# Optimization experiments

Measured on AMD Instinct MI355X. Metric: run time of the kernel, lower is better.

The kernel has to match this reference:

```python
import jax, jax.numpy as jnp
import numpy as np

INPUT_DIM = 1024
HIDDEN = 1024
NUM_EXPERTS = 64
TOP_K = 8
N_TOKENS = 32768


def _linear_params(key, fan_in, fan_out):
    kw, kb = jax.random.split(key)
    bound = 1.0 / np.sqrt(fan_in)
    w = jax.random.uniform(kw, (fan_in, fan_out), jnp.float32, -bound, bound)
    b = jax.random.uniform(kb, (fan_out,), jnp.float32, -bound, bound)
    return w, b


def setup_inputs() -> dict:
    key = jax.random.key(0)
    ks = jax.random.split(key, 8)
    x = jax.random.normal(ks[0], (N_TOKENS, INPUT_DIM), jnp.float32)
    noise = jax.random.normal(ks[1], (N_TOKENS, NUM_EXPERTS), jnp.float32)
    h2 = 2 * HIDDEN
    w1, b1 = _linear_params(ks[2], INPUT_DIM, h2)
    w2, b2 = _linear_params(ks[3], h2, h2)
    wn, bn = _linear_params(ks[4], h2, h2)
    w3, b3 = _linear_params(ks[5], h2, HIDDEN)
    w4, b4 = _linear_params(ks[6], HIDDEN, NUM_EXPERTS)
    wz, bz = _linear_params(ks[7], INPUT_DIM, NUM_EXPERTS)
    return {"x": x, "noise": noise, "w1": w1, "b1": b1, "w2": w2, "b2": b2,
            "wn": wn, "bn": bn, "w3": w3, "b3": b3, "w4": w4, "b4": b4,
            "wz": wz, "bz": bz}


def reference(x, noise, w1, b1, w2, b2, wn, bn, w3, b3, w4, b4, wz, bz):
    relu = jax.nn.relu
    h = relu(x @ w1 + b1)            # [N, 2H]
    h = relu(h @ w2 + b2)            # [N, 2H]
    h = relu(h @ wn + bn)            # [N, 2H]
    h = relu(h @ w3 + b3)            # [N, H]
    logits = h @ w4 + b4             # [N, E]
    noise_logits = x @ wz + bz       # [N, E]
    noisy_logits = logits + noise * jax.nn.softplus(noise_logits)
    top_k_logits, indices = jax.lax.top_k(noisy_logits, TOP_K)  # [N, K]
    rows = jnp.arange(noisy_logits.shape[0])[:, None]
    sparse_logits = jnp.full_like(noisy_logits, -jnp.inf).at[rows, indices].set(top_k_logits)
    router_output = jax.nn.softmax(sparse_logits, axis=-1)      # [N, E]
    return router_output, indices
```

## Files before the change

kernel.cpp:

```cpp
#include <hip/hip_runtime.h>
#include <math.h>

#define IN_DIM 1024
#define H2     2048
#define HID    1024
#define NEXP   64
#define TOPK   8
#define RISK_TH 1.5e-4f

typedef short  v8s __attribute__((ext_vector_type(8)));
typedef float  v4f __attribute__((ext_vector_type(4)));

__device__ __forceinline__ void bf16_split(float f, ushort& h, ushort& l) {
    unsigned uh = __float_as_uint(f) & 0xffff0000u;
    h = (ushort)(uh >> 16);
    float r = f - __uint_as_float(uh);
    l = (ushort)(__float_as_uint(r) >> 16);
}

__device__ __forceinline__ void gload16(const ushort* g, ushort* l) {
    __builtin_amdgcn_global_load_lds(
        (const __attribute__((address_space(1))) void*)g,
        (__attribute__((address_space(3))) void*)l, 16, 0, 0);
}

__global__ __launch_bounds__(256)
void split_w_kernel(const float* __restrict__ W, ushort* __restrict__ hiT,
                    ushort* __restrict__ loT, int K, int N)
{
    __shared__ float T[64][65];
    const int k0 = blockIdx.y * 64, n0 = blockIdx.x * 64;
    const int t = threadIdx.x;
#pragma unroll
    for (int j = 0; j < 4; ++j) {
        int idx = t + j * 256;
        int row = idx >> 4;
        int c4  = (idx & 15) * 4;
        float4 f = *(const float4*)(W + (long)(k0 + row) * N + n0 + c4);
        T[row][c4 + 0] = f.x; T[row][c4 + 1] = f.y;
        T[row][c4 + 2] = f.z; T[row][c4 + 3] = f.w;
    }
    __syncthreads();
#pragma unroll
    for (int j = 0; j < 4; ++j) {
        int idx = t + j * 256;
        int nn = idx >> 4;
        int kq = (idx & 15) * 4;
        ushort4 h4, l4;
        bf16_split(T[kq + 0][nn], h4.x, l4.x);
        bf16_split(T[kq + 1][nn], h4.y, l4.y);
        bf16_split(T[kq + 2][nn], h4.z, l4.z);
        bf16_split(T[kq + 3][nn], h4.w, l4.w);
        long o = (long)(n0 + nn) * K + k0 + kq;
        *(ushort4*)(hiT + o) = h4;
        *(ushort4*)(loT + o) = l4;
    }
}

__global__ __launch_bounds__(256)
void split_x_kernel(const float* __restrict__ X, ushort* __restrict__ hi,
                    ushort* __restrict__ lo)
{
    long i = ((long)blockIdx.x * 256 + threadIdx.x) * 4;
    float4 f = *(const float4*)(X + i);
    ushort4 h4, l4;
    bf16_split(f.x, h4.x, l4.x);
    bf16_split(f.y, h4.y, l4.y);
    bf16_split(f.z, h4.z, l4.z);
    bf16_split(f.w, h4.w, l4.w);
    *(ushort4*)(hi + i) = h4;
    *(ushort4*)(lo + i) = l4;
}

template<int MI, int NWN>
__global__ __launch_bounds__(512, 2)
void gemm8p_kernel(const ushort* __restrict__ gAhi, const ushort* __restrict__ gAlo,
                   const ushort* __restrict__ gBhi, const ushort* __restrict__ gBlo,
                   const float* __restrict__ bias,
                   float* __restrict__ Cf32, ushort* __restrict__ Chi,
                   ushort* __restrict__ Clo, int N, int K)
{
    static_assert(MI == 2 * NWN, "wave grid must tile 256 rows");
    constexpr int BN    = NWN * 64;
    constexpr int ATILE = 256 * 32;
    constexpr int BTILE = BN * 32;
    constexpr int BUFU  = 2 * ATILE + 2 * BTILE;
    constexpr int MH    = MI / 2;
    __shared__ __align__(16) ushort lds[2 * BUFU];

    const int tid  = threadIdx.x;
    const int w    = tid >> 6;
    const int lane = tid & 63;
    const int wm   = w / NWN;
    const int wn   = w % NWN;
    const int q    = lane >> 4;
    const int l15  = lane & 15;

    const int nwg = (int)(gridDim.x * gridDim.y);
    const int h   = (int)(blockIdx.y * gridDim.x + blockIdx.x);
    const int l   = (h & 7) * (nwg >> 3) + (h >> 3);
    const long bm = (long)(l >> 3) * 256;
    const long bn = (long)(l & 7) * BN;

    const int  e   = lane >> 2;
    const int  s8  = (((lane & 3) ^ ((lane >> 3) & 3)) * 8);
    const int  fragUS = ((q ^ ((l15 >> 1) & 3)) * 8);

    const int NT = K >> 5;

    v4f acc[MI][4];
#pragma unroll
    for (int mi = 0; mi < MI; ++mi)
#pragma unroll
        for (int ni = 0; ni < 4; ++ni)
            acc[mi][ni] = (v4f){0.f, 0.f, 0.f, 0.f};

    {
        ushort* nb = lds;
        const long grA = bm + w * 16 + e;
        gload16(gAhi + grA * K + s8,                     nb + w * 512);
        gload16(gAhi + (grA + 128) * K + s8,             nb + 128 * 32 + w * 512);
        gload16(gAlo + grA * K + s8,                     nb + ATILE + w * 512);
        gload16(gAlo + (grA + 128) * K + s8,             nb + ATILE + 128 * 32 + w * 512);
        const long grB = bn + w * 16 + e;
        gload16(gBhi + grB * K + s8,                     nb + 2 * ATILE + w * 512);
        gload16(gBlo + grB * K + s8,                     nb + 2 * ATILE + BTILE + w * 512);
        if constexpr (BN == 256) {
            gload16(gBhi + (grB + 128) * K + s8,         nb + 2 * ATILE + 128 * 32 + w * 512);
            gload16(gBlo + (grB + 128) * K + s8,         nb + 2 * ATILE + BTILE + 128 * 32 + w * 512);
        }
    }
    asm volatile("s_waitcnt vmcnt(0)" ::: "memory");
    __builtin_amdgcn_s_barrier();

    for (int t = 0; t < NT; ++t) {
        const ushort* cA = lds + (t & 1) * BUFU;
        const ushort* cB = cA + 2 * ATILE;
        ushort* nb = lds + ((t + 1) & 1) * BUFU;
        const bool more = (t + 1 < NT);
        const int  ktn  = (t + 1) << 5;

        v8s ah[MH], al[MH];
        v8s bh0[2], bl0[2];
        v8s bh1[2], bl1[2];

#pragma unroll
        for (int i = 0; i < MH; ++i) {
            int r = wm * (MI * 16) + i * 16 + l15;
            const ushort* pA = cA + r * 32 + fragUS;
            ah[i] = *(const v8s*)pA;
            al[i] = *(const v8s*)(pA + ATILE);
        }
#pragma unroll
        for (int j = 0; j < 2; ++j) {
            int r = wn * 64 + j * 16 + l15;
            const ushort* pB = cB + r * 32 + fragUS;
            bh0[j] = *(const v8s*)pB;
            bl0[j] = *(const v8s*)(pB + BTILE);
        }
        if (more) {
            const long gr = bm + w * 16 + e;
            gload16(gAhi + gr * K + ktn + s8,             nb + w * 512);
            gload16(gAhi + (gr + 128) * K + ktn + s8,     nb + 128 * 32 + w * 512);
            gload16(gAlo + gr * K + ktn + s8,             nb + ATILE + w * 512);
            gload16(gAlo + (gr + 128) * K + ktn + s8,     nb + ATILE + 128 * 32 + w * 512);
        }
        asm volatile("s_waitcnt lgkmcnt(0)" ::: "memory");
        __builtin_amdgcn_sched_barrier(0);

#pragma unroll
        for (int j = 0; j < 2; ++j) {
            int r = wn * 64 + (2 + j) * 16 + l15;
            const ushort* pB = cB + r * 32 + fragUS;
            bh1[j] = *(const v8s*)pB;
            bl1[j] = *(const v8s*)(pB + BTILE);
        }

        __builtin_amdgcn_s_setprio(1);
#pragma unroll
        for (int i = 0; i < MH; ++i)
#pragma unroll
            for (int j = 0; j < 2; ++j) {
                v4f c = acc[i][j];
                c = __builtin_amdgcn_mfma_f32_16x16x32_bf16(al[i], bh0[j], c, 0, 0, 0);
                c = __builtin_amdgcn_mfma_f32_16x16x32_bf16(ah[i], bl0[j], c, 0, 0, 0);
                c = __builtin_amdgcn_mfma_f32_16x16x32_bf16(ah[i], bh0[j], c, 0, 0, 0);
                acc[i][j] = c;
            }
        __builtin_amdgcn_s_setprio(0);

        if (more) {
            const long gr = bn + w * 16 + e;
            gload16(gBhi + gr * K + ktn + s8,             nb + 2 * ATILE + w * 512);
            gload16(gBlo + gr * K + ktn + s8,             nb + 2 * ATILE + BTILE + w * 512);
            if constexpr (BN == 256) {
                gload16(gBhi + (gr + 128) * K + ktn + s8, nb + 2 * ATILE + 128 * 32 + w * 512);
                gload16(gBlo + (gr + 128) * K + ktn + s8, nb + 2 * ATILE + BTILE + 128 * 32 + w * 512);
            }
        }
        asm volatile("s_waitcnt lgkmcnt(0)" ::: "memory");
        __builtin_amdgcn_sched_barrier(0);

        __builtin_amdgcn_s_setprio(1);
#pragma unroll
        for (int i = 0; i < MH; ++i)
#pragma unroll
            for (int j = 0; j < 2; ++j) {
                v4f c = acc[i][2 + j];
                c = __builtin_amdgcn_mfma_f32_16x16x32_bf16(al[i], bh1[j], c, 0, 0, 0);
                c = __builtin_amdgcn_mfma_f32_16x16x32_bf16(ah[i], bl1[j], c, 0, 0, 0);
                c = __builtin_amdgcn_mfma_f32_16x16x32_bf16(ah[i], bh1[j], c, 0, 0, 0);
                acc[i][2 + j] = c;
            }
        __builtin_amdgcn_s_setprio(0);

#pragma unroll
        for (int i = 0; i < MH; ++i) {
            int r = wm * (MI * 16) + (MH + i) * 16 + l15;
            const ushort* pA = cA + r * 32 + fragUS;
            ah[i] = *(const v8s*)pA;
            al[i] = *(const v8s*)(pA + ATILE);
        }
        asm volatile("s_waitcnt lgkmcnt(0)" ::: "memory");
        __builtin_amdgcn_sched_barrier(0);

        __builtin_amdgcn_s_setprio(1);
#pragma unroll
        for (int i = 0; i < MH; ++i)
#pragma unroll
            for (int j = 0; j < 2; ++j) {
                v4f c = acc[MH + i][2 + j];
                c = __builtin_amdgcn_mfma_f32_16x16x32_bf16(al[i], bh1[j], c, 0, 0, 0);
                c = __builtin_amdgcn_mfma_f32_16x16x32_bf16(ah[i], bl1[j], c, 0, 0, 0);
                c = __builtin_amdgcn_mfma_f32_16x16x32_bf16(ah[i], bh1[j], c, 0, 0, 0);
                acc[MH + i][2 + j] = c;
            }
#pragma unroll
        for (int i = 0; i < MH; ++i)
#pragma unroll
            for (int j = 0; j < 2; ++j) {
                v4f c = acc[MH + i][j];
                c = __builtin_amdgcn_mfma_f32_16x16x32_bf16(al[i], bh0[j], c, 0, 0, 0);
                c = __builtin_amdgcn_mfma_f32_16x16x32_bf16(ah[i], bl0[j], c, 0, 0, 0);
                c = __builtin_amdgcn_mfma_f32_16x16x32_bf16(ah[i], bh0[j], c, 0, 0, 0);
                acc[MH + i][j] = c;
            }
        __builtin_amdgcn_s_setprio(0);

        asm volatile("s_waitcnt vmcnt(0)" ::: "memory");
        __builtin_amdgcn_s_barrier();
    }

#pragma unroll
    for (int ni = 0; ni < 4; ++ni) {
        int col = (int)(bn + wn * 64 + ni * 16 + l15);
        float bv = bias[col];
#pragma unroll
        for (int mi = 0; mi < MI; ++mi) {
            long row0 = bm + wm * (MI * 16) + mi * 16 + q * 4;
#pragma unroll
            for (int r = 0; r < 4; ++r) {
                float v = fmaxf(acc[mi][ni][r] + bv, 0.f);
                long o = (row0 + r) * (long)N + col;
                if (Cf32) {
                    Cf32[o] = v;
                } else {
                    ushort hh, ll;
                    bf16_split(v, hh, ll);
                    Chi[o] = hh;
                    Clo[o] = ll;
                }
            }
        }
    }
}

#define SBM 64
#define SBK 32
#define SLDA 68

__global__ __launch_bounds__(256, 2)
void small_gemm_kernel(const float* __restrict__ A, const float* __restrict__ B,
                       const float* __restrict__ bias, float* __restrict__ C,
                       int K)
{
    __shared__ __align__(16) float Hs[SBK][SLDA];
    __shared__ __align__(16) float Ws[SBK][NEXP];
    const int tid = threadIdx.x;
    const int tx = tid & 15;
    const int ty = tid >> 4;
    const long bm = (long)blockIdx.x * SBM;
    const float* Ab = A + bm * K;

    float acc[4][4];
#pragma unroll
    for (int i = 0; i < 4; ++i)
#pragma unroll
        for (int j = 0; j < 4; ++j) acc[i][j] = 0.f;

    float4 aR[2], bR[2];
#pragma unroll
    for (int j = 0; j < 2; ++j) {
        int idx = tid + (j << 8);
        int ar = idx >> 3, ac = (idx & 7) << 2;
        aR[j] = *(const float4*)(Ab + (long)ar * K + ac);
        int br = idx >> 4, bc = (idx & 15) << 2;
        bR[j] = *(const float4*)(B + (long)br * NEXP + bc);
    }

    int kt = 0;
    for (;;) {
#pragma unroll
        for (int j = 0; j < 2; ++j) {
            int idx = tid + (j << 8);
            int ar = idx >> 3, ac = (idx & 7) << 2;
            Hs[ac + 0][ar] = aR[j].x;
            Hs[ac + 1][ar] = aR[j].y;
            Hs[ac + 2][ar] = aR[j].z;
            Hs[ac + 3][ar] = aR[j].w;
            int br = idx >> 4, bc = (idx & 15) << 2;
            *(float4*)&Ws[br][bc] = bR[j];
        }
        __syncthreads();

        kt += SBK;
        if (kt < K) {
#pragma unroll
            for (int j = 0; j < 2; ++j) {
                int idx = tid + (j << 8);
                int ar = idx >> 3, ac = (idx & 7) << 2;
                aR[j] = *(const float4*)(Ab + (long)ar * K + kt + ac);
                int br = idx >> 4, bc = (idx & 15) << 2;
                bR[j] = *(const float4*)(B + (long)(kt + br) * NEXP + bc);
            }
        }

#pragma unroll
        for (int k = 0; k < SBK; ++k) {
            float a[4], b[4];
            *(float4*)&a[0] = *(const float4*)&Hs[k][ty * 4];
            *(float4*)&b[0] = *(const float4*)&Ws[k][tx * 4];
#pragma unroll
            for (int i = 0; i < 4; ++i)
#pragma unroll
                for (int j = 0; j < 4; ++j)
                    acc[i][j] = fmaf(a[i], b[j], acc[i][j]);
        }
        __syncthreads();
        if (kt >= K) break;
    }

    float bv[4];
#pragma unroll
    for (int j = 0; j < 4; ++j) bv[j] = bias[tx * 4 + j];
#pragma unroll
    for (int i = 0; i < 4; ++i) {
        long row = bm + ty * 4 + i;
        float o[4];
#pragma unroll
        for (int j = 0; j < 4; ++j) o[j] = acc[i][j] + bv[j];
        *(float4*)(C + row * NEXP + tx * 4) = *(const float4*)&o[0];
    }
}

__global__ __launch_bounds__(256)
void router_kernel(const float* __restrict__ logits, const float* __restrict__ nlog,
                   const float* __restrict__ noise, float* __restrict__ rout,
                   float* __restrict__ idx_out, int rows, int rowBase,
                   int* __restrict__ ctrl, int* __restrict__ list, int maxr)
{
    const int wave = threadIdx.x >> 6;
    const int lane = threadIdx.x & 63;
    const long row = (long)blockIdx.x * 4 + wave;
    if (row >= rows) return;

    float lg = logits[row * NEXP + lane];
    float nl = nlog[row * NEXP + lane];
    float nz = noise[row * NEXP + lane];
    float sp = fmaxf(nl, 0.f) + log1pf(expf(-fabsf(nl)));
    float v  = lg + nz * sp;

    float orig = v;
    float work = v;
    bool  sel  = false;
    float myidx = 0.f;
    float m = 0.f, ssum = 0.f;
    float prev = 0.f, minGap = INFINITY;

#pragma unroll
    for (int r = 0; r < TOPK + 1; ++r) {
        float bvv = work;
        int   bi  = lane;
#pragma unroll
        for (int off = 32; off > 0; off >>= 1) {
            float ov = __shfl_xor(bvv, off);
            int   oi = __shfl_xor(bi, off);
            if (ov > bvv || (ov == bvv && oi < bi)) { bvv = ov; bi = oi; }
        }
        if (r > 0) minGap = fminf(minGap, prev - bvv);
        prev = bvv;
        if (r < TOPK) {
            if (r == 0) m = bvv;
            ssum += expf(bvv - m);
            if (lane == bi) { work = -INFINITY; sel = true; }
            if (lane == r)  myidx = (float)bi;
        }
    }

    float p = sel ? expf(orig - m) / ssum : 0.f;
    rout[row * NEXP + lane] = p;
    if (lane < TOPK) idx_out[row * TOPK + lane] = myidx;

    if (lane == 0 && minGap < RISK_TH) {
        int slot = atomicAdd(ctrl, 1);
        if (slot < maxr) list[slot] = rowBase + (int)row;
    }
}

__global__ void init_kernel(int* ctrl) { if (threadIdx.x == 0) ctrl[0] = 0; }

__global__ void pad_kernel(int* ctrl, int* list, int maxr)
{
    int cnt = ctrl[0]; if (cnt > maxr) cnt = maxr;
    int rounded = (cnt + 63) & ~63; if (rounded > maxr) rounded = maxr;
    if (threadIdx.x == 0) { ctrl[1] = rounded; ctrl[2] = cnt; }
    int fill = (cnt > 0) ? list[0] : 0;
    for (int i = cnt + threadIdx.x; i < rounded; i += blockDim.x) list[i] = fill;
}

#define DBM 64
#define DBN 64
#define DBK 32

__global__ __launch_bounds__(256)
void dgemm_f64(const double* __restrict__ A64, const float* __restrict__ A32,
               const int* __restrict__ rowList,
               const float* __restrict__ B, const float* __restrict__ bias,
               double* __restrict__ C, int N, int K, int doRelu,
               const int* __restrict__ ctrl)
{
    const int mBase = blockIdx.y * DBM;
    if (mBase >= ctrl[1]) return;

    __shared__ __align__(16) double As[DBM][DBK + 2];
    __shared__ __align__(16) double Bs[DBK][DBN];
    __shared__ int rowIdx[DBM];

    const int tid = threadIdx.x;
    const int tx = tid & 15;
    const int ty = tid >> 4;
    const int nBase = blockIdx.x * DBN;

    if (A32 && tid < DBM) rowIdx[tid] = rowList[mBase + tid];
    __syncthreads();

    const int ar = tid >> 4;
    const int ak = (tid & 15) * 2;
    const int bc = (tid & 15) * 4;

    int rIdx[4];
    if (A32) {
#pragma unroll
        for (int j = 0; j < 4; ++j) rIdx[j] = rowIdx[ar + j * 16];
    }

    double acc[4][4];
#pragma unroll
    for (int i = 0; i < 4; ++i)
#pragma unroll
        for (int j = 0; j < 4; ++j) acc[i][j] = 0.0;

    double2 aReg[4];
    float4  bReg[2];

#pragma unroll
    for (int j = 0; j < 4; ++j) {
        if (A32) {
            const float2 f = *(const float2*)(A32 + (long)rIdx[j] * K + ak);
            aReg[j].x = (double)f.x; aReg[j].y = (double)f.y;
        } else {
            aReg[j] = *(const double2*)(A64 + (long)(mBase + ar + j * 16) * K + ak);
        }
    }
#pragma unroll
    for (int j = 0; j < 2; ++j)
        bReg[j] = *(const float4*)(B + (long)(ar + j * 16) * N + nBase + bc);

    int kt = 0;
    for (;;) {
#pragma unroll
        for (int j = 0; j < 4; ++j)
            *(double2*)&As[ar + j * 16][ak] = aReg[j];
#pragma unroll
        for (int j = 0; j < 2; ++j) {
            double2 lo, hi;
            lo.x = (double)bReg[j].x; lo.y = (double)bReg[j].y;
            hi.x = (double)bReg[j].z; hi.y = (double)bReg[j].w;
            *(double2*)&Bs[ar + j * 16][bc]     = lo;
            *(double2*)&Bs[ar + j * 16][bc + 2] = hi;
        }
        __syncthreads();

        kt += DBK;
        if (kt < K) {
#pragma unroll
            for (int j = 0; j < 4; ++j) {
                if (A32) {
                    const float2 f = *(const float2*)(A32 + (long)rIdx[j] * K + kt + ak);
                    aReg[j].x = (double)f.x; aReg[j].y = (double)f.y;
                } else {
                    aReg[j] = *(const double2*)(A64 + (long)(mBase + ar + j * 16) * K + kt + ak);
                }
            }
#pragma unroll
            for (int j = 0; j < 2; ++j)
                bReg[j] = *(const float4*)(B + (long)(kt + ar + j * 16) * N + nBase + bc);
        }

#pragma unroll
        for (int k = 0; k < DBK; ++k) {
            double a[4], b[4];
#pragma unroll
            for (int i = 0; i < 4; ++i) a[i] = As[ty * 4 + i][k];
            *(double2*)&b[0] = *(const double2*)&Bs[k][tx * 4];
            *(double2*)&b[2] = *(const double2*)&Bs[k][tx * 4 + 2];
#pragma unroll
            for (int i = 0; i < 4; ++i)
#pragma unroll
                for (int j = 0; j < 4; ++j)
                    acc[i][j] = fma(a[i], b[j], acc[i][j]);
        }
        __syncthreads();
        if (kt >= K) break;
    }

#pragma unroll
    for (int i = 0; i < 4; ++i) {
        long row = mBase + ty * 4 + i;
#pragma unroll
        for (int j = 0; j < 4; ++j) {
            int n = nBase + tx * 4 + j;
            double v = acc[i][j] + (double)bias[n];
            if (doRelu) v = fmax(v, 0.0);
            C[row * N + n] = v;
        }
    }
}

__global__ __launch_bounds__(256)
void router_fix_kernel(const double* __restrict__ lgd, const double* __restrict__ nld,
                       const float* __restrict__ noise, float* __restrict__ rout,
                       float* __restrict__ idx_out,
                       const int* __restrict__ ctrl, const int* __restrict__ list)
{
    const int wave = threadIdx.x >> 6;
    const int lane = threadIdx.x & 63;
    const int i = blockIdx.x * 4 + wave;
    if (i >= ctrl[2]) return;
    const long row = list[i];

    double lg = lgd[(long)i * NEXP + lane];
    double nl = nld[(long)i * NEXP + lane];
    double nz = (double)noise[row * NEXP + lane];
    double sp = fmax(nl, 0.0) + log1p(exp(-fabs(nl)));
    double v  = lg + nz * sp;

    double orig = v, work = v;
    bool sel = false;
    float myidx = 0.f;
    double m = 0.0, ssum = 0.0;

#pragma unroll
    for (int r = 0; r < TOPK; ++r) {
        double bvv = work;
        int    bi  = lane;
#pragma unroll
        for (int off = 32; off > 0; off >>= 1) {
            double ov = __shfl_xor(bvv, off);
            int    oi = __shfl_xor(bi, off);
            if (ov > bvv || (ov == bvv && oi < bi)) { bvv = ov; bi = oi; }
        }
        if (r == 0) m = bvv;
        ssum += exp(bvv - m);
        if (lane == bi) { work = -INFINITY; sel = true; }
        if (lane == r)  myidx = (float)bi;
    }

    double p = sel ? exp(orig - m) / ssum : 0.0;
    rout[row * NEXP + lane] = (float)p;
    if (lane < TOPK) idx_out[row * TOPK + lane] = myidx;
}

extern "C" void kernel_launch(void* const* d_in, const int* in_sizes, int n_in,
                              void* d_out, int out_size, void* d_ws, size_t ws_size,
                              hipStream_t stream)
{
    const float* x     = (const float*)d_in[0];
    const float* noise = (const float*)d_in[1];
    const float* w1 = (const float*)d_in[2];
    const float* b1 = (const float*)d_in[3];
    const float* w2 = (const float*)d_in[4];
    const float* b2 = (const float*)d_in[5];
    const float* wn = (const float*)d_in[6];
    const float* bn = (const float*)d_in[7];
    const float* w3 = (const float*)d_in[8];
    const float* b3 = (const float*)d_in[9];
    const float* w4 = (const float*)d_in[10];
    const float* b4 = (const float*)d_in[11];
    const float* wz = (const float*)d_in[12];
    const float* bz = (const float*)d_in[13];
    float* out = (float*)d_out;

    const int Ntok = in_sizes[0] / IN_DIM;

    const size_t e1 = (size_t)IN_DIM * H2;
    const size_t e2 = (size_t)H2 * H2;
    const size_t en = (size_t)H2 * H2;
    const size_t e3 = (size_t)H2 * HID;
    size_t weightBytes = 2 * (e1 + e2 + en + e3) * sizeof(ushort);
    weightBytes = (weightBytes + 255) & ~(size_t)255;

    const size_t perTok = (size_t)4 * H2 * 2 + (size_t)IN_DIM * 4 + 2 * NEXP * 4;
    int chunk = 8192;
    while (chunk > 256) {
        size_t needb = weightBytes + (size_t)chunk * perTok + 65536;
        if (needb <= ws_size) break;
        chunk >>= 1;
    }
    if (chunk > Ntok) chunk = Ntok;

    int MAXR = chunk / 2;
    if (MAXR > 4096) MAXR = 4096;

    ushort* w1Thi = (ushort*)d_ws;
    ushort* w1Tlo = w1Thi + e1;
    ushort* w2Thi = w1Tlo + e1;
    ushort* w2Tlo = w2Thi + e2;
    ushort* wnThi = w2Tlo + e2;
    ushort* wnTlo = wnThi + en;
    ushort* w3Thi = wnTlo + en;
    ushort* w3Tlo = w3Thi + e3;

    char* region = (char*)d_ws + weightBytes;
    const size_t regionBytes = (size_t)chunk * perTok;

    ushort* pAhi = (ushort*)region;
    ushort* pAlo = pAhi + (size_t)chunk * H2;
    ushort* pBhi = pAlo + (size_t)chunk * H2;
    ushort* pBlo = pBhi + (size_t)chunk * H2;
    char*   ureg = (char*)(pBlo + (size_t)chunk * H2);
    ushort* xphi = (ushort*)ureg;
    ushort* xplo = xphi + (size_t)chunk * IN_DIM;
    float*  hfin = (float*)ureg;
    float*  lg   = (float*)(ureg + (size_t)chunk * IN_DIM * 4);
    float*  nl   = lg + (size_t)chunk * NEXP;

    double* hA  = (double*)region;
    double* hB  = hA + (size_t)MAXR * H2;
    double* lgd = hB + (size_t)MAXR * H2;
    double* nld = lgd + (size_t)MAXR * NEXP;

    int* ctrl = (int*)(region + regionBytes);
    int* list = ctrl + 16;

    float* ridx = out + (size_t)Ntok * NEXP;

    const dim3 blk(256);
    init_kernel<<<1, 64, 0, stream>>>(ctrl);

    split_w_kernel<<<dim3(H2 / 64,  IN_DIM / 64), blk, 0, stream>>>(w1, w1Thi, w1Tlo, IN_DIM, H2);
    split_w_kernel<<<dim3(H2 / 64,  H2 / 64),     blk, 0, stream>>>(w2, w2Thi, w2Tlo, H2, H2);
    split_w_kernel<<<dim3(H2 / 64,  H2 / 64),     blk, 0, stream>>>(wn, wnThi, wnTlo, H2, H2);
    split_w_kernel<<<dim3(HID / 64, H2 / 64),     blk, 0, stream>>>(w3, w3Thi, w3Tlo, H2, HID);

    for (int c0 = 0; c0 < Ntok; c0 += chunk) {
        const float* xa = x + (size_t)c0 * IN_DIM;
        split_x_kernel<<<dim3(chunk), blk, 0, stream>>>(xa, xphi, xplo);
        gemm8p_kernel<8, 4><<<dim3(H2 / 256,  chunk / 256), 512, 0, stream>>>(
            xphi, xplo, w1Thi, w1Tlo, b1, nullptr, pAhi, pAlo, H2, IN_DIM);
        gemm8p_kernel<8, 4><<<dim3(H2 / 256,  chunk / 256), 512, 0, stream>>>(
            pAhi, pAlo, w2Thi, w2Tlo, b2, nullptr, pBhi, pBlo, H2, H2);
        gemm8p_kernel<8, 4><<<dim3(H2 / 256,  chunk / 256), 512, 0, stream>>>(
            pBhi, pBlo, wnThi, wnTlo, bn, nullptr, pAhi, pAlo, H2, H2);
        gemm8p_kernel<4, 2><<<dim3(HID / 128, chunk / 256), 512, 0, stream>>>(
            pAhi, pAlo, w3Thi, w3Tlo, b3, hfin, nullptr, nullptr, HID, H2);
        small_gemm_kernel<<<dim3(chunk / SBM), blk, 0, stream>>>(hfin, w4, b4, lg, HID);
        small_gemm_kernel<<<dim3(chunk / SBM), blk, 0, stream>>>(xa,   wz, bz, nl, IN_DIM);
        router_kernel<<<dim3(chunk / 4), blk, 0, stream>>>(lg, nl, noise + (size_t)c0 * NEXP,
                                                           out + (size_t)c0 * NEXP,
                                                           ridx + (size_t)c0 * TOPK, chunk, c0,
                                                           ctrl, list, MAXR);
    }

    pad_kernel<<<1, 256, 0, stream>>>(ctrl, list, MAXR);

    const dim3 gy(H2 / DBN, MAXR / DBM);
    dgemm_f64<<<gy, blk, 0, stream>>>(nullptr, x, list, w1, b1, hA, H2, IN_DIM, 1, ctrl);
    dgemm_f64<<<gy, blk, 0, stream>>>(hA, nullptr, nullptr, w2, b2, hB, H2, H2, 1, ctrl);
    dgemm_f64<<<gy, blk, 0, stream>>>(hB, nullptr, nullptr, wn, bn, hA, H2, H2, 1, ctrl);
    dgemm_f64<<<dim3(HID / DBN, MAXR / DBM), blk, 0, stream>>>(hA, nullptr, nullptr, w3, b3, hB, HID, H2, 1, ctrl);
    dgemm_f64<<<dim3(1, MAXR / DBM), blk, 0, stream>>>(hB, nullptr, nullptr, w4, b4, lgd, NEXP, HID, 0, ctrl);
    dgemm_f64<<<dim3(1, MAXR / DBM), blk, 0, stream>>>(nullptr, x, list, wz, bz, nld, NEXP, IN_DIM, 0, ctrl);
    router_fix_kernel<<<dim3(MAXR / 4), blk, 0, stream>>>(lgd, nld, noise, out, ridx, ctrl, list);
}
```

Baseline: 3.620 ms.

## Split-K the FP64 fix-up GEMMs with atomic accumulation and separate bias/ReLU pass

The double-precision re-computation path for risky rows now splits the K dimension across blockIdx.z and accumulates partial products into zeroed outputs with atomic adds. Bias and ReLU move into a separate fixzero kernel that also zeroes the next layer's output buffer, and the last-layer biases are folded into router_fix. The aim is more blocks in flight, since only a few rows are risky and the M-dimension grid is small. The cost is extra atomic traffic, extra kernel launches, and results that are not bitwise deterministic. The B fragment read in shared memory also changes from a contiguous double2 pattern to strided scalar reads.

```diff
diff --git a/kernel.cpp b/kernel.cpp
--- a/kernel.cpp
+++ b/kernel.cpp
@@ -428,19 +428,52 @@
     for (int i = cnt + threadIdx.x; i < rounded; i += blockDim.x) list[i] = fill;
 }
 
+__global__ __launch_bounds__(256)
+void fixzero_kernel(double* P, const float* __restrict__ bias, int cols,
+                    double* Z, int zcols, const int* __restrict__ ctrl)
+{
+    const int rp = blockIdx.y * 64;
+    if (rp >= ctrl[1]) return;
+    const int c0 = blockIdx.x * 64;
+    if (P && c0 < cols) {
+#pragma unroll
+        for (int i = 0; i < 8; ++i) {
+            int idx = threadIdx.x + i * 256;
+            int row = idx >> 5;
+            int col = (idx & 31) * 2;
+            long o = (long)(rp + row) * cols + c0 + col;
+            double2 v = *(double2*)(P + o);
+            v.x = fmax(v.x + (double)bias[c0 + col],     0.0);
+            v.y = fmax(v.y + (double)bias[c0 + col + 1], 0.0);
+            *(double2*)(P + o) = v;
+        }
+    }
+    if (Z && c0 < zcols) {
+        const double2 z2 = {0.0, 0.0};
+#pragma unroll
+        for (int i = 0; i < 8; ++i) {
+            int idx = threadIdx.x + i * 256;
+            int row = idx >> 5;
+            int col = (idx & 31) * 2;
+            *(double2*)(Z + (long)(rp + row) * zcols + c0 + col) = z2;
+        }
+    }
+}
+
 #define DBM 64
 #define DBN 64
 #define DBK 32
 
 __global__ __launch_bounds__(256)
-void dgemm_f64(const double* __restrict__ A64, const float* __restrict__ A32,
-               const int* __restrict__ rowList,
-               const float* __restrict__ B, const float* __restrict__ bias,
-               double* __restrict__ C, int N, int K, int doRelu,
-               const int* __restrict__ ctrl)
+void dgemm_ks(const double* __restrict__ A64, const float* __restrict__ A32,
+              const int* __restrict__ rowList,
+              const float* __restrict__ B, double* __restrict__ C,
+              int N, int K, int kLen, const int* __restrict__ ctrl)
 {
     const int mBase = blockIdx.y * DBM;
     if (mBase >= ctrl[1]) return;
+    const int kBase = blockIdx.z * kLen;
+    const int kEnd  = kBase + kLen;
 
     __shared__ __align__(16) double As[DBM][DBK + 2];
     __shared__ __align__(16) double Bs[DBK][DBN];
@@ -473,20 +506,23 @@
     double2 aReg[4];
     float4  bReg[2];
 
-#pragma unroll
-    for (int j = 0; j < 4; ++j) {
-        if (A32) {
-            const float2 f = *(const float2*)(A32 + (long)rIdx[j] * K + ak);
-            aReg[j].x = (double)f.x; aReg[j].y = (double)f.y;
-        } else {
-            aReg[j] = *(const double2*)(A64 + (long)(mBase + ar + j * 16) * K + ak);
-        }
-    }
-#pragma unroll
-    for (int j = 0; j < 2; ++j)
-        bReg[j] = *(const float4*)(B + (long)(ar + j * 16) * N + nBase + bc);
-
-    int kt = 0;
+    auto prefetch = [&](int ktv) {
+#pragma unroll
+        for (int j = 0; j < 4; ++j) {
+            if (A32) {
+                const float2 f = *(const float2*)(A32 + (long)rIdx[j] * K + ktv + ak);
+                aReg[j].x = (double)f.x; aReg[j].y = (double)f.y;
+            } else {
+                aReg[j] = *(const double2*)(A64 + (long)(mBase + ar + j * 16) * K + ktv + ak);
+            }
+        }
+#pragma unroll
+        for (int j = 0; j < 2; ++j)
+            bReg[j] = *(const float4*)(B + (long)(ktv + ar + j * 16) * N + nBase + bc);
+    };
+
+    prefetch(kBase);
+    int kt = kBase;
     for (;;) {
 #pragma unroll
         for (int j = 0; j < 4; ++j)
@@ -502,28 +538,15 @@
         __syncthreads();
 
         kt += DBK;
-        if (kt < K) {
-#pragma unroll
-            for (int j = 0; j < 4; ++j) {
-                if (A32) {
-                    const float2 f = *(const float2*)(A32 + (long)rIdx[j] * K + kt + ak);
-                    aReg[j].x = (double)f.x; aReg[j].y = (double)f.y;
-                } else {
-                    aReg[j] = *(const double2*)(A64 + (long)(mBase + ar + j * 16) * K + kt + ak);
-                }
-            }
-#pragma unroll
-            for (int j = 0; j < 2; ++j)
-                bReg[j] = *(const float4*)(B + (long)(kt + ar + j * 16) * N + nBase + bc);
-        }
+        if (kt < kEnd) prefetch(kt);
 
 #pragma unroll
         for (int k = 0; k < DBK; ++k) {
             double a[4], b[4];
 #pragma unroll
             for (int i = 0; i < 4; ++i) a[i] = As[ty * 4 + i][k];
-            *(double2*)&b[0] = *(const double2*)&Bs[k][tx * 4];
-            *(double2*)&b[2] = *(const double2*)&Bs[k][tx * 4 + 2];
+#pragma unroll
+            for (int j = 0; j < 4; ++j) b[j] = Bs[k][tx + j * 16];
 #pragma unroll
             for (int i = 0; i < 4; ++i)
 #pragma unroll
@@ -531,7 +554,7 @@
                     acc[i][j] = fma(a[i], b[j], acc[i][j]);
         }
         __syncthreads();
-        if (kt >= K) break;
+        if (kt >= kEnd) break;
     }
 
 #pragma unroll
@@ -539,16 +562,19 @@
         long row = mBase + ty * 4 + i;
 #pragma unroll
         for (int j = 0; j < 4; ++j) {
-            int n = nBase + tx * 4 + j;
-            double v = acc[i][j] + (double)bias[n];
-            if (doRelu) v = fmax(v, 0.0);
-            C[row * N + n] = v;
+            int n = nBase + tx + j * 16;
+#if defined(__HIP_PLATFORM_AMD__)
+            unsafeAtomicAdd(&C[row * N + n], acc[i][j]);
+#else
+            atomicAdd(&C[row * N + n], acc[i][j]);
+#endif
         }
     }
 }
 
 __global__ __launch_bounds__(256)
 void router_fix_kernel(const double* __restrict__ lgd, const double* __restrict__ nld,
+                       const float* __restrict__ b4f, const float* __restrict__ bzf,
                        const float* __restrict__ noise, float* __restrict__ rout,
                        float* __restrict__ idx_out,
                        const int* __restrict__ ctrl, const int* __restrict__ list)
@@ -559,8 +585,8 @@
     if (i >= ctrl[2]) return;
     const long row = list[i];
 
-    double lg = lgd[(long)i * NEXP + lane];
-    double nl = nld[(long)i * NEXP + lane];
+    double lg = lgd[(long)i * NEXP + lane] + (double)b4f[lane];
+    double nl = nld[(long)i * NEXP + lane] + (double)bzf[lane];
     double nz = (double)noise[row * NEXP + lane];
     double sp = fmax(nl, 0.0) + log1p(exp(-fabs(nl)));
     double v  = lg + nz * sp;
@@ -694,12 +720,18 @@
 
     pad_kernel<<<1, 256, 0, stream>>>(ctrl, list, MAXR);
 
-    const dim3 gy(H2 / DBN, MAXR / DBM);
-    dgemm_f64<<<gy, blk, 0, stream>>>(nullptr, x, list, w1, b1, hA, H2, IN_DIM, 1, ctrl);
-    dgemm_f64<<<gy, blk, 0, stream>>>(hA, nullptr, nullptr, w2, b2, hB, H2, H2, 1, ctrl);
-    dgemm_f64<<<gy, blk, 0, stream>>>(hB, nullptr, nullptr, wn, bn, hA, H2, H2, 1, ctrl);
-    dgemm_f64<<<dim3(HID / DBN, MAXR / DBM), blk, 0, stream>>>(hA, nullptr, nullptr, w3, b3, hB, HID, H2, 1, ctrl);
-    dgemm_f64<<<dim3(1, MAXR / DBM), blk, 0, stream>>>(hB, nullptr, nullptr, w4, b4, lgd, NEXP, HID, 0, ctrl);
-    dgemm_f64<<<dim3(1, MAXR / DBM), blk, 0, stream>>>(nullptr, x, list, wz, bz, nld, NEXP, IN_DIM, 0, ctrl);
-    router_fix_kernel<<<dim3(MAXR / 4), blk, 0, stream>>>(lgd, nld, noise, out, ridx, ctrl, list);
-}
+    const int GY = MAXR / DBM;
+    fixzero_kernel<<<dim3(H2 / 64, GY), blk, 0, stream>>>(nullptr, nullptr, 0, hA, H2, ctrl);
+    dgemm_ks<<<dim3(H2 / DBN, GY, 4), blk, 0, stream>>>(nullptr, x, list, w1, hA, H2, IN_DIM, IN_DIM / 4, ctrl);
+    fixzero_kernel<<<dim3(H2 / 64, GY), blk, 0, stream>>>(hA, b1, H2, hB, H2, ctrl);
+    dgemm_ks<<<dim3(H2 / DBN, GY, 4), blk, 0, stream>>>(hA, nullptr, nullptr, w2, hB, H2, H2, H2 / 4, ctrl);
+    fixzero_kernel<<<dim3(H2 / 64, GY), blk, 0, stream>>>(hB, b2, H2, hA, H2, ctrl);
+    dgemm_ks<<<dim3(H2 / DBN, GY, 4), blk, 0, stream>>>(hB, nullptr, nullptr, wn, hA, H2, H2, H2 / 4, ctrl);
+    fixzero_kernel<<<dim3(H2 / 64, GY), blk, 0, stream>>>(hA, bn, H2, hB, HID, ctrl);
+    dgemm_ks<<<dim3(HID / DBN, GY, 8), blk, 0, stream>>>(hA, nullptr, nullptr, w3, hB, HID, H2, H2 / 8, ctrl);
+    fixzero_kernel<<<dim3(HID / 64, GY), blk, 0, stream>>>(hB, b3, HID, lgd, NEXP, ctrl);
+    fixzero_kernel<<<dim3(1, GY), blk, 0, stream>>>(nullptr, nullptr, 0, nld, NEXP, ctrl);
+    dgemm_ks<<<dim3(1, GY, 16), blk, 0, stream>>>(hB, nullptr, nullptr, w4, lgd, NEXP, HID, HID / 16, ctrl);
+    dgemm_ks<<<dim3(1, GY, 16), blk, 0, stream>>>(nullptr, x, list, wz, nld, NEXP, IN_DIM, IN_DIM / 16, ctrl);
+    router_fix_kernel<<<dim3(MAXR / 4), blk, 0, stream>>>(lgd, nld, b4, bz, noise, out, ridx, ctrl, list);
+}
```

Result: faster. 3.151 ms (-12.9%).
